# Kernel optimization log

Measured on AMD Instinct MI355X. Metric: run time of the kernel, lower is better.

## Reference

```python
import jax, jax.numpy as jnp
import numpy as np

B, W, C, H = 2, 2048, 1024, 16
K = C // H  # 64
LN_EPS = 1e-5


def setup_inputs() -> dict:
    key = jax.random.key(0)
    ks = jax.random.split(key, 8)
    return {
        "seq1": jax.random.normal(ks[0], (B, W, C), jnp.float32),
        "seq2": jax.random.normal(ks[1], (B, W, C), jnp.float32),
        "ln_gamma": jnp.ones((C,), jnp.float32),
        "ln_beta": jnp.zeros((C,), jnp.float32),
        "q_proj": jax.random.normal(ks[2], (H, C, K), jnp.float32) * 0.02,
        "k_proj": jax.random.normal(ks[3], (H, C, K), jnp.float32) * 0.02,
        "v_proj": jax.random.normal(ks[4], (H, C, K), jnp.float32) * 0.02,
        "mixer_w": jax.random.normal(ks[5], (C, C), jnp.float32) * 0.02,
        "mixer_b": jnp.zeros((C,), jnp.float32),
    }


def _layernorm(x, gamma, beta):
    mu = jnp.mean(x, axis=-1, keepdims=True)
    var = jnp.mean(jnp.square(x - mu), axis=-1, keepdims=True)
    return (x - mu) * jax.lax.rsqrt(var + LN_EPS) * gamma + beta


def reference(seq1, seq2, ln_gamma, ln_beta, q_proj, k_proj, v_proj, mixer_w, mixer_b):
    x1 = _layernorm(seq1, ln_gamma, ln_beta)  # [B,W,C]
    x2 = _layernorm(seq2, ln_gamma, ln_beta)
    # per-head projections: [B,W,C] x [H,C,K] -> [B,H,W,K]
    q = jnp.einsum("bwc,hck->bhwk", x1, q_proj)
    k = jnp.einsum("bwc,hck->bhwk", x2, k_proj)
    v = jnp.einsum("bwc,hck->bhwk", x2, v_proj)
    scores = jnp.einsum("bhqk,bhmk->bhqm", q, k) / jnp.sqrt(jnp.float32(K))
    # causal mask (is_decoder=True)
    causal = jnp.tril(jnp.ones((W, W), bool))
    scores = jnp.where(causal[None, None], scores, jnp.float32(-jnp.inf))
    probs = jax.nn.softmax(scores, axis=-1)
    out = jnp.einsum("bhqm,bhmk->bhqk", probs, v)  # [B,H,W,K]
    out = out.transpose(0, 2, 1, 3).reshape(B, W, C)  # [B,W,C]
    return out @ mixer_w.T + mixer_b
```

## Files before the change

kernel.cpp:

```cpp
#include <hip/hip_runtime.h>
#include <math.h>

#define B_ 2
#define W_ 2048
#define C_ 1024
#define H_ 16
#define K_ 64
#define LN_EPS 1e-5f

typedef __attribute__((ext_vector_type(8))) short short8;
typedef __attribute__((ext_vector_type(4))) float float4v;

#if __has_builtin(__builtin_amdgcn_exp2f)
#define EXP2(x) __builtin_amdgcn_exp2f(x)
#else
#define EXP2(x) exp2f(x)
#endif

__device__ inline unsigned short f2bf(float f) {
  unsigned u = __float_as_uint(f);
  u += 0x7fffu + ((u >> 16) & 1u);
  return (unsigned short)(u >> 16);
}

__device__ __forceinline__ void gload_lds16(const short* g, short* l) {
  __builtin_amdgcn_global_load_lds(
      (const __attribute__((address_space(1))) void*)g,
      (__attribute__((address_space(3))) void*)l, 16, 0, 0);
}

__device__ inline float block_sum(float val) {
  __shared__ float sb[4];
  #pragma unroll
  for (int o = 32; o > 0; o >>= 1) val += __shfl_down(val, o, 64);
  int lane = threadIdx.x & 63, wid = threadIdx.x >> 6;
  if (lane == 0) sb[wid] = val;
  __syncthreads();
  float r = sb[0] + sb[1] + sb[2] + sb[3];
  __syncthreads();
  return r;
}

__global__ __launch_bounds__(256) void ln_kernel(
    const float* __restrict__ seq1, const float* __restrict__ seq2,
    const float* __restrict__ gamma, const float* __restrict__ beta,
    short* __restrict__ x1b, short* __restrict__ x2b) {
  int row = blockIdx.x;
  const int nrows = B_ * W_;
  bool first = row < nrows;
  const float* src = first ? seq1 : seq2;
  short* dst = first ? x1b : x2b;
  int r = first ? row : row - nrows;

  const float4* p = (const float4*)(src + (size_t)r * C_);
  float4 v = p[threadIdx.x];
  float mean = block_sum(v.x + v.y + v.z + v.w) * (1.0f / C_);
  float dx = v.x - mean, dy = v.y - mean, dz = v.z - mean, dw = v.w - mean;
  float var = block_sum(dx * dx + dy * dy + dz * dz + dw * dw) * (1.0f / C_);
  float rstd = rsqrtf(var + LN_EPS);

  float4 g = ((const float4*)gamma)[threadIdx.x];
  float4 b = ((const float4*)beta)[threadIdx.x];
  uint2 o;
  o.x = (unsigned)f2bf(dx * rstd * g.x + b.x) |
        ((unsigned)f2bf(dy * rstd * g.y + b.y) << 16);
  o.y = (unsigned)f2bf(dz * rstd * g.z + b.z) |
        ((unsigned)f2bf(dw * rstd * g.w + b.w) << 16);
  ((uint2*)(dst + (size_t)r * C_))[threadIdx.x] = o;
}

__global__ __launch_bounds__(256) void wprep_proj_kernel(
    const float* __restrict__ qp, const float* __restrict__ kp,
    const float* __restrict__ vp,
    short* __restrict__ wqt, short* __restrict__ wkt, short* __restrict__ wvt) {
  int cb = blockIdx.x, h = blockIdx.y, which = blockIdx.z;
  const float* P = (which == 0 ? qp : (which == 1 ? kp : vp)) + (size_t)h * C_ * K_;
  short* Wt = (which == 0 ? wqt : (which == 1 ? wkt : wvt));
  float scale = (which == 0) ? 0.125f * 1.4426950408889634f : 1.0f;

  __shared__ float Ls[64][65];
  int t = threadIdx.x;
  {
    int cr = t >> 2, ks = (t & 3) * 16;
    const float* src = P + (size_t)(cb * 64 + cr) * K_ + ks;
    #pragma unroll
    for (int j = 0; j < 4; ++j) {
      float4 v = *(const float4*)(src + j * 4);
      Ls[cr][ks + j * 4 + 0] = v.x; Ls[cr][ks + j * 4 + 1] = v.y;
      Ls[cr][ks + j * 4 + 2] = v.z; Ls[cr][ks + j * 4 + 3] = v.w;
    }
  }
  __syncthreads();
  int kr = t >> 2, cs = (t & 3) * 16;
  unsigned u[8];
  #pragma unroll
  for (int i = 0; i < 8; ++i) {
    float a = Ls[cs + 2 * i][kr] * scale;
    float b = Ls[cs + 2 * i + 1][kr] * scale;
    u[i] = (unsigned)f2bf(a) | ((unsigned)f2bf(b) << 16);
  }
  short* dst = Wt + ((size_t)h * 64 + kr) * C_ + cb * 64 + cs;
  uint4 p0; p0.x = u[0]; p0.y = u[1]; p0.z = u[2]; p0.w = u[3];
  uint4 p1; p1.x = u[4]; p1.y = u[5]; p1.z = u[6]; p1.w = u[7];
  *(uint4*)dst = p0;
  *(uint4*)(dst + 8) = p1;
}

__global__ __launch_bounds__(256) void wprep_mix_kernel(
    const float* __restrict__ wm, short* __restrict__ wmb) {
  int gid = blockIdx.x * 256 + threadIdx.x;
  float4 v = ((const float4*)wm)[gid];
  uint2 o;
  o.x = (unsigned)f2bf(v.x) | ((unsigned)f2bf(v.y) << 16);
  o.y = (unsigned)f2bf(v.z) | ((unsigned)f2bf(v.w) << 16);
  ((uint2*)wmb)[gid] = o;
}

__device__ __forceinline__ void gemm_core(
    const short* __restrict__ A, const short* __restrict__ Bt,
    int arow0, int brow0, short* As, short* Bs, float4v acc[4][4]) {
  int tid = threadIdx.x;
  int wave = tid >> 6, lane = tid & 63;
  int lr = lane >> 3, lc = lane & 7;
  int sc = lc ^ lr;
  int wr = wave >> 1, wc = wave & 1;
  int lg = lane >> 4, ll = lane & 15;

  #pragma unroll
  for (int mi = 0; mi < 4; ++mi)
    #pragma unroll
    for (int ni = 0; ni < 4; ++ni) {
      acc[mi][ni][0] = 0.f; acc[mi][ni][1] = 0.f;
      acc[mi][ni][2] = 0.f; acc[mi][ni][3] = 0.f;
    }

  for (int k0 = 0; k0 < C_; k0 += 64) {
    __syncthreads();
    #pragma unroll
    for (int j = 0; j < 4; ++j) {
      int seg = wave * 4 + j;
      int r = seg * 8 + lr;
      gload_lds16(A + (size_t)(arow0 + r) * C_ + k0 + sc * 8, As + seg * 512);
      gload_lds16(Bt + (size_t)(brow0 + r) * C_ + k0 + sc * 8, Bs + seg * 512);
    }
    __syncthreads();
    #pragma unroll
    for (int kc = 0; kc < 2; ++kc) {
      int cc = kc * 4 + lg;
      short8 af[4], bf[4];
      #pragma unroll
      for (int mi = 0; mi < 4; ++mi) {
        int m = wr * 64 + mi * 16 + ll;
        af[mi] = *(const short8*)&As[m * 64 + ((cc ^ (m & 7)) << 3)];
      }
      #pragma unroll
      for (int ni = 0; ni < 4; ++ni) {
        int n = wc * 64 + ni * 16 + ll;
        bf[ni] = *(const short8*)&Bs[n * 64 + ((cc ^ (n & 7)) << 3)];
      }
      #pragma unroll
      for (int mi = 0; mi < 4; ++mi)
        #pragma unroll
        for (int ni = 0; ni < 4; ++ni)
          acc[mi][ni] = __builtin_amdgcn_mfma_f32_16x16x32_bf16(
              af[mi], bf[ni], acc[mi][ni], 0, 0, 0);
    }
  }
}

__device__ __forceinline__ void gemm_core64(
    const short* __restrict__ A, const short* __restrict__ Bt,
    int arow0, int brow0, short* As, short* Bs, float4v acc[2][4]) {
  int tid = threadIdx.x;
  int wave = tid >> 6, lane = tid & 63;
  int lr = lane >> 3, lc = lane & 7;
  int sc = lc ^ lr;
  int wr = wave >> 1, wc = wave & 1;
  int lg = lane >> 4, ll = lane & 15;

  #pragma unroll
  for (int mi = 0; mi < 2; ++mi)
    #pragma unroll
    for (int ni = 0; ni < 4; ++ni) {
      acc[mi][ni][0] = 0.f; acc[mi][ni][1] = 0.f;
      acc[mi][ni][2] = 0.f; acc[mi][ni][3] = 0.f;
    }

  for (int k0 = 0; k0 < C_; k0 += 64) {
    __syncthreads();
    #pragma unroll
    for (int j = 0; j < 2; ++j) {
      int seg = wave * 2 + j;
      int r = seg * 8 + lr;
      gload_lds16(A + (size_t)(arow0 + r) * C_ + k0 + sc * 8, As + seg * 512);
    }
    #pragma unroll
    for (int j = 0; j < 4; ++j) {
      int seg = wave * 4 + j;
      int r = seg * 8 + lr;
      gload_lds16(Bt + (size_t)(brow0 + r) * C_ + k0 + sc * 8, Bs + seg * 512);
    }
    __syncthreads();
    #pragma unroll
    for (int kc = 0; kc < 2; ++kc) {
      int cc = kc * 4 + lg;
      short8 af[2], bf[4];
      #pragma unroll
      for (int mi = 0; mi < 2; ++mi) {
        int m = wr * 32 + mi * 16 + ll;
        af[mi] = *(const short8*)&As[m * 64 + ((cc ^ (m & 7)) << 3)];
      }
      #pragma unroll
      for (int ni = 0; ni < 4; ++ni) {
        int n = wc * 64 + ni * 16 + ll;
        bf[ni] = *(const short8*)&Bs[n * 64 + ((cc ^ (n & 7)) << 3)];
      }
      #pragma unroll
      for (int mi = 0; mi < 2; ++mi)
        #pragma unroll
        for (int ni = 0; ni < 4; ++ni)
          acc[mi][ni] = __builtin_amdgcn_mfma_f32_16x16x32_bf16(
              af[mi], bf[ni], acc[mi][ni], 0, 0, 0);
    }
  }
}

__global__ __launch_bounds__(256, 3) void gemm_qkv_kernel(
    const short* __restrict__ x1b, const short* __restrict__ x2b,
    const short* __restrict__ wqt, const short* __restrict__ wkt,
    const short* __restrict__ wvt,
    short* __restrict__ qb, short* __restrict__ kb, short* __restrict__ vtb) {
  __shared__ short As[128 * 64], Bs[128 * 64];
  int z = blockIdx.z;
  const short *A, *Bt;
  int arow0, brow0;
  if (z == 0)      { A = x1b; Bt = wqt; arow0 = blockIdx.x * 128; brow0 = blockIdx.y * 128; }
  else if (z == 1) { A = x2b; Bt = wkt; arow0 = blockIdx.x * 128; brow0 = blockIdx.y * 128; }
  else             { A = wvt; Bt = x2b; arow0 = blockIdx.y * 128; brow0 = blockIdx.x * 128; }

  float4v acc[4][4];
  gemm_core(A, Bt, arow0, brow0, As, Bs, acc);

  int wave = threadIdx.x >> 6, lane = threadIdx.x & 63;
  int wr = wave >> 1, wc = wave & 1, lg = lane >> 4, ll = lane & 15;
  if (z <= 1) {
    short* O = (z == 0) ? qb : kb;
    #pragma unroll
    for (int mi = 0; mi < 4; ++mi)
      #pragma unroll
      for (int ni = 0; ni < 4; ++ni) {
        int n = brow0 + wc * 64 + ni * 16 + ll;
        int h = n >> 6, kk = n & 63;
        #pragma unroll
        for (int r2 = 0; r2 < 4; ++r2) {
          int m = arow0 + wr * 64 + mi * 16 + lg * 4 + r2;
          int b = m >> 11, w = m & (W_ - 1);
          O[((size_t)(b * H_ + h) * W_ + w) * K_ + kk] = (short)f2bf(acc[mi][ni][r2]);
        }
      }
  } else {
    #pragma unroll
    for (int mi = 0; mi < 4; ++mi)
      #pragma unroll
      for (int ni = 0; ni < 4; ++ni) {
        int n = brow0 + wc * 64 + ni * 16 + ll;
        int b = n >> 11, w = n & (W_ - 1);
        #pragma unroll
        for (int r2 = 0; r2 < 4; ++r2) {
          int m = arow0 + wr * 64 + mi * 16 + lg * 4 + r2;
          int h = m >> 6, kk = m & 63;
          vtb[((size_t)(b * H_ + h) * K_ + kk) * W_ + w] = (short)f2bf(acc[mi][ni][r2]);
        }
      }
  }
}

__global__ __launch_bounds__(256, 3) void gemm_mix_kernel(
    const short* __restrict__ attnb, const short* __restrict__ wmb,
    const float* __restrict__ bias, float* __restrict__ out) {
  __shared__ short As[64 * 64], Bs[128 * 64];
  int arow0 = blockIdx.x * 64, brow0 = blockIdx.y * 128;
  float4v acc[2][4];
  gemm_core64(attnb, wmb, arow0, brow0, As, Bs, acc);

  int wave = threadIdx.x >> 6, lane = threadIdx.x & 63;
  int wr = wave >> 1, wc = wave & 1, lg = lane >> 4, ll = lane & 15;
  #pragma unroll
  for (int mi = 0; mi < 2; ++mi)
    #pragma unroll
    for (int ni = 0; ni < 4; ++ni) {
      int n = brow0 + wc * 64 + ni * 16 + ll;
      float bv = bias[n];
      #pragma unroll
      for (int r2 = 0; r2 < 4; ++r2) {
        int m = arow0 + wr * 32 + mi * 16 + lg * 4 + r2;
        out[(size_t)m * C_ + n] = acc[mi][ni][r2] + bv;
      }
    }
}

__global__ __launch_bounds__(256, 3) void attn_mfma_kernel(
    const short* __restrict__ q, const short* __restrict__ k,
    const short* __restrict__ vt, short* __restrict__ out) {
  int bh = blockIdx.x;
  int b = bh >> 4, h = bh & 15;
  int s = blockIdx.y;
  int qt = (s < 16) ? (31 - s) : (s - 16);
  int wave = threadIdx.x >> 6;
  int lane = threadIdx.x & 63;
  int lg = lane >> 4, ll = lane & 15;

  __shared__ short Ks[2][64 * 64];
  __shared__ short Vs[2][64 * 64];
  __shared__ short Ps[4][16 * 72];

  const short* qp = q + (size_t)bh * W_ * K_;
  const short* kp = k + (size_t)bh * W_ * K_;
  const short* vb = vt + (size_t)bh * K_ * W_;

  int qrow = qt * 64 + wave * 16 + ll;
  short8 aq[2];
  #pragma unroll
  for (int kc = 0; kc < 2; ++kc)
    aq[kc] = *(const short8*)(qp + (size_t)qrow * K_ + kc * 32 + lg * 8);

  float4v o[4];
  #pragma unroll
  for (int ct = 0; ct < 4; ++ct) {
    o[ct][0] = 0.f; o[ct][1] = 0.f; o[ct][2] = 0.f; o[ct][3] = 0.f;
  }
  float m = -INFINITY, l = 0.f;

  int nkt = qt + 1;

  #define STAGE(kt, buf)                                                   \
    {                                                                      \
      const short* kbase = kp + (size_t)(kt) * 64 * K_;                    \
      const short* vbase = vb + (kt) * 64;                                 \
      _Pragma("unroll")                                                    \
      for (int j = 0; j < 2; ++j) {                                        \
        int sdx = j * 256 + (int)threadIdx.x;                              \
        int mm = sdx >> 3, c7 = sdx & 7;                                   \
        int gc = c7 ^ (mm & 7);                                            \
        gload_lds16(kbase + (size_t)mm * K_ + gc * 8, &Ks[buf][sdx * 8]);  \
        gload_lds16(vbase + (size_t)mm * W_ + gc * 8, &Vs[buf][sdx * 8]);  \
      }                                                                    \
    }

  STAGE(0, 0);
  for (int kt = 0; kt < nkt; ++kt) {
    int cur = kt & 1;
    if (kt + 1 < nkt) {
      STAGE(kt + 1, cur ^ 1);
      asm volatile("s_waitcnt vmcnt(4)\ns_barrier" ::: "memory");
    } else {
      asm volatile("s_waitcnt vmcnt(0)\ns_barrier" ::: "memory");
    }

    float4v st[4];
    #pragma unroll
    for (int nt = 0; nt < 4; ++nt) {
      st[nt][0] = 0.f; st[nt][1] = 0.f; st[nt][2] = 0.f; st[nt][3] = 0.f;
      int n = nt * 16 + ll;
      #pragma unroll
      for (int kc = 0; kc < 2; ++kc) {
        int cc = kc * 4 + lg;
        short8 bk = *(const short8*)&Ks[cur][n * 64 + ((cc ^ (n & 7)) << 3)];
        st[nt] = __builtin_amdgcn_mfma_f32_16x16x32_bf16(bk, aq[kc], st[nt], 0, 0, 0);
      }
    }
    short8 bv[4][2];
    #pragma unroll
    for (int ct = 0; ct < 4; ++ct) {
      int c = ct * 16 + ll;
      #pragma unroll
      for (int kc = 0; kc < 2; ++kc) {
        int cc = kc * 4 + lg;
        bv[ct][kc] = *(const short8*)&Vs[cur][c * 64 + ((cc ^ (c & 7)) << 3)];
      }
    }

    if (kt == qt) {
      #pragma unroll
      for (int nt = 0; nt < 4; ++nt) {
        int keyb = nt * 16 + lg * 4;
        #pragma unroll
        for (int r = 0; r < 4; ++r)
          if (keyb + r > wave * 16 + ll) st[nt][r] = -INFINITY;
      }
    }

    float mx0 = fmaxf(fmaxf(st[0][0], st[0][1]), fmaxf(st[0][2], st[0][3]));
    float mx1 = fmaxf(fmaxf(st[1][0], st[1][1]), fmaxf(st[1][2], st[1][3]));
    float mx2 = fmaxf(fmaxf(st[2][0], st[2][1]), fmaxf(st[2][2], st[2][3]));
    float mx3 = fmaxf(fmaxf(st[3][0], st[3][1]), fmaxf(st[3][2], st[3][3]));
    float lm = fmaxf(fmaxf(mx0, mx1), fmaxf(mx2, mx3));
    lm = fmaxf(lm, __shfl_xor(lm, 16, 64));
    lm = fmaxf(lm, __shfl_xor(lm, 32, 64));
    if (!__all(lm <= m + 8.f)) {
      float nm = fmaxf(m, lm);
      float al = EXP2(m - nm);
      m = nm;
      l *= al;
      #pragma unroll
      for (int ct = 0; ct < 4; ++ct) {
        o[ct][0] *= al; o[ct][1] *= al; o[ct][2] *= al; o[ct][3] *= al;
      }
    }
    float p[4][4];
    #pragma unroll
    for (int nt = 0; nt < 4; ++nt)
      #pragma unroll
      for (int r = 0; r < 4; ++r)
        p[nt][r] = EXP2(st[nt][r] - m);
    float s0 = (p[0][0] + p[0][1]) + (p[0][2] + p[0][3]);
    float s1 = (p[1][0] + p[1][1]) + (p[1][2] + p[1][3]);
    float s2 = (p[2][0] + p[2][1]) + (p[2][2] + p[2][3]);
    float s3 = (p[3][0] + p[3][1]) + (p[3][2] + p[3][3]);
    float ps = (s0 + s1) + (s2 + s3);
    ps += __shfl_xor(ps, 16, 64);
    ps += __shfl_xor(ps, 32, 64);
    l += ps;

    short* myP = &Ps[wave][ll * 72];
    #pragma unroll
    for (int nt = 0; nt < 4; ++nt) {
      uint2 w;
      w.x = (unsigned)f2bf(p[nt][0]) | ((unsigned)f2bf(p[nt][1]) << 16);
      w.y = (unsigned)f2bf(p[nt][2]) | ((unsigned)f2bf(p[nt][3]) << 16);
      *(uint2*)(myP + nt * 16 + lg * 4) = w;
    }
    __builtin_amdgcn_s_waitcnt(0xC07F);
    short8 bp0 = *(const short8*)(myP + lg * 8);
    short8 bp1 = *(const short8*)(myP + 32 + lg * 8);
    #pragma unroll
    for (int ct = 0; ct < 4; ++ct) {
      o[ct] = __builtin_amdgcn_mfma_f32_16x16x32_bf16(bv[ct][0], bp0, o[ct], 0, 0, 0);
      o[ct] = __builtin_amdgcn_mfma_f32_16x16x32_bf16(bv[ct][1], bp1, o[ct], 0, 0, 0);
    }
    asm volatile("s_waitcnt lgkmcnt(0)\ns_barrier" ::: "memory");
  }
  #undef STAGE

  float invl = 1.0f / l;
  size_t orow = ((size_t)(b * W_ + qrow)) * C_ + h * K_;
  #pragma unroll
  for (int ct = 0; ct < 4; ++ct) {
    uint2 w;
    w.x = (unsigned)f2bf(o[ct][0] * invl) | ((unsigned)f2bf(o[ct][1] * invl) << 16);
    w.y = (unsigned)f2bf(o[ct][2] * invl) | ((unsigned)f2bf(o[ct][3] * invl) << 16);
    *(uint2*)(out + orow + ct * 16 + lg * 4) = w;
  }
}

extern "C" void kernel_launch(void* const* d_in, const int* in_sizes, int n_in,
                              void* d_out, int out_size, void* d_ws, size_t ws_size,
                              hipStream_t stream) {
  const float* seq1  = (const float*)d_in[0];
  const float* seq2  = (const float*)d_in[1];
  const float* gamma = (const float*)d_in[2];
  const float* beta  = (const float*)d_in[3];
  const float* qp    = (const float*)d_in[4];
  const float* kp    = (const float*)d_in[5];
  const float* vp    = (const float*)d_in[6];
  const float* wm    = (const float*)d_in[7];
  const float* mb    = (const float*)d_in[8];
  float* out = (float*)d_out;

  char* ws = (char*)d_ws;
  const size_t NROW = (size_t)B_ * W_;
  const size_t XB = NROW * C_ * sizeof(short);
  const size_t WB = (size_t)C_ * C_ * sizeof(short);
  short* x1b = (short*)(ws);
  short* x2b = (short*)(ws + XB);
  short* qb  = (short*)(ws + 2 * XB);
  short* kb  = (short*)(ws + 3 * XB);
  short* vtb = (short*)(ws + 4 * XB);
  short* wqt = (short*)(ws + 5 * XB);
  short* wkt = (short*)(ws + 5 * XB + WB);
  short* wvt = (short*)(ws + 5 * XB + 2 * WB);
  short* wmb = (short*)(ws + 5 * XB + 3 * WB);
  short* attnb = (short*)(ws + 5 * XB + 4 * WB);

  wprep_proj_kernel<<<dim3(C_ / 64, H_, 3), dim3(256), 0, stream>>>(
      qp, kp, vp, wqt, wkt, wvt);
  wprep_mix_kernel<<<dim3(C_ * C_ / 1024), dim3(256), 0, stream>>>(wm, wmb);
  ln_kernel<<<dim3(2 * (unsigned)NROW), dim3(256), 0, stream>>>(
      seq1, seq2, gamma, beta, x1b, x2b);
  gemm_qkv_kernel<<<dim3(32, 8, 3), dim3(256), 0, stream>>>(
      x1b, x2b, wqt, wkt, wvt, qb, kb, vtb);
  attn_mfma_kernel<<<dim3(32, 32), dim3(256), 0, stream>>>(
      qb, kb, vtb, attnb);
  gemm_mix_kernel<<<dim3(64, 8), dim3(256), 0, stream>>>(attnb, wmb, mb, out);
}
```

Baseline: 192.7 us.

## Compute softmax row sums via MFMA with ones, add setprio and max3 reductions

Replaces the scalar per-tile row-sum and its cross-lane shuffles with two extra MFMAs that multiply a ones matrix by the bf16 probability tile, accumulating the denominator in matrix-core registers. Also wraps the MFMA sections in s_setprio to favour matrix issue across waves, and restructures the row-max into three-input max operations. The row sum now uses bf16-rounded probabilities, which matches what is fed to the PV product but changes numerics slightly, and it adds matrix-core work per tile.

```diff
diff --git a/kernel.cpp b/kernel.cpp
--- a/kernel.cpp
+++ b/kernel.cpp
@@ -21,6 +21,10 @@
   unsigned u = __float_as_uint(f);
   u += 0x7fffu + ((u >> 16) & 1u);
   return (unsigned short)(u >> 16);
+}
+
+__device__ inline float max3f(float a, float b, float c) {
+  return fmaxf(fmaxf(a, b), c);
 }
 
 __device__ __forceinline__ void gload_lds16(const short* g, short* l) {
@@ -324,12 +328,18 @@
   for (int kc = 0; kc < 2; ++kc)
     aq[kc] = *(const short8*)(qp + (size_t)qrow * K_ + kc * 32 + lg * 8);
 
+  short8 ones;
+  #pragma unroll
+  for (int i = 0; i < 8; ++i) ones[i] = (short)0x3F80;
+
   float4v o[4];
   #pragma unroll
   for (int ct = 0; ct < 4; ++ct) {
     o[ct][0] = 0.f; o[ct][1] = 0.f; o[ct][2] = 0.f; o[ct][3] = 0.f;
   }
-  float m = -INFINITY, l = 0.f;
+  float4v lsum;
+  lsum[0] = 0.f; lsum[1] = 0.f; lsum[2] = 0.f; lsum[3] = 0.f;
+  float m = -INFINITY;
 
   int nkt = qt + 1;
 
@@ -358,6 +368,7 @@
     }
 
     float4v st[4];
+    __builtin_amdgcn_s_setprio(1);
     #pragma unroll
     for (int nt = 0; nt < 4; ++nt) {
       st[nt][0] = 0.f; st[nt][1] = 0.f; st[nt][2] = 0.f; st[nt][3] = 0.f;
@@ -369,6 +380,8 @@
         st[nt] = __builtin_amdgcn_mfma_f32_16x16x32_bf16(bk, aq[kc], st[nt], 0, 0, 0);
       }
     }
+    __builtin_amdgcn_s_setprio(0);
+
     short8 bv[4][2];
     #pragma unroll
     for (int ct = 0; ct < 4; ++ct) {
@@ -390,37 +403,31 @@
       }
     }
 
-    float mx0 = fmaxf(fmaxf(st[0][0], st[0][1]), fmaxf(st[0][2], st[0][3]));
-    float mx1 = fmaxf(fmaxf(st[1][0], st[1][1]), fmaxf(st[1][2], st[1][3]));
-    float mx2 = fmaxf(fmaxf(st[2][0], st[2][1]), fmaxf(st[2][2], st[2][3]));
-    float mx3 = fmaxf(fmaxf(st[3][0], st[3][1]), fmaxf(st[3][2], st[3][3]));
-    float lm = fmaxf(fmaxf(mx0, mx1), fmaxf(mx2, mx3));
+    float ma = max3f(st[0][0], st[0][1], st[0][2]);
+    float mb = max3f(st[0][3], st[1][0], st[1][1]);
+    float mc = max3f(st[1][2], st[1][3], st[2][0]);
+    float md = max3f(st[2][1], st[2][2], st[2][3]);
+    float me = max3f(st[3][0], st[3][1], st[3][2]);
+    float lm = fmaxf(max3f(ma, mb, mc), max3f(md, me, st[3][3]));
     lm = fmaxf(lm, __shfl_xor(lm, 16, 64));
     lm = fmaxf(lm, __shfl_xor(lm, 32, 64));
     if (!__all(lm <= m + 8.f)) {
       float nm = fmaxf(m, lm);
       float al = EXP2(m - nm);
       m = nm;
-      l *= al;
+      lsum[0] *= al; lsum[1] *= al; lsum[2] *= al; lsum[3] *= al;
       #pragma unroll
       for (int ct = 0; ct < 4; ++ct) {
         o[ct][0] *= al; o[ct][1] *= al; o[ct][2] *= al; o[ct][3] *= al;
       }
     }
+
     float p[4][4];
     #pragma unroll
     for (int nt = 0; nt < 4; ++nt)
       #pragma unroll
       for (int r = 0; r < 4; ++r)
         p[nt][r] = EXP2(st[nt][r] - m);
-    float s0 = (p[0][0] + p[0][1]) + (p[0][2] + p[0][3]);
-    float s1 = (p[1][0] + p[1][1]) + (p[1][2] + p[1][3]);
-    float s2 = (p[2][0] + p[2][1]) + (p[2][2] + p[2][3]);
-    float s3 = (p[3][0] + p[3][1]) + (p[3][2] + p[3][3]);
-    float ps = (s0 + s1) + (s2 + s3);
-    ps += __shfl_xor(ps, 16, 64);
-    ps += __shfl_xor(ps, 32, 64);
-    l += ps;
 
     short* myP = &Ps[wave][ll * 72];
     #pragma unroll
@@ -433,16 +440,21 @@
     __builtin_amdgcn_s_waitcnt(0xC07F);
     short8 bp0 = *(const short8*)(myP + lg * 8);
     short8 bp1 = *(const short8*)(myP + 32 + lg * 8);
+
+    __builtin_amdgcn_s_setprio(1);
+    lsum = __builtin_amdgcn_mfma_f32_16x16x32_bf16(ones, bp0, lsum, 0, 0, 0);
+    lsum = __builtin_amdgcn_mfma_f32_16x16x32_bf16(ones, bp1, lsum, 0, 0, 0);
     #pragma unroll
     for (int ct = 0; ct < 4; ++ct) {
       o[ct] = __builtin_amdgcn_mfma_f32_16x16x32_bf16(bv[ct][0], bp0, o[ct], 0, 0, 0);
       o[ct] = __builtin_amdgcn_mfma_f32_16x16x32_bf16(bv[ct][1], bp1, o[ct], 0, 0, 0);
     }
+    __builtin_amdgcn_s_setprio(0);
     asm volatile("s_waitcnt lgkmcnt(0)\ns_barrier" ::: "memory");
   }
   #undef STAGE
 
-  float invl = 1.0f / l;
+  float invl = 1.0f / lsum[0];
   size_t orow = ((size_t)(b * W_ + qrow)) * C_ + h * K_;
   #pragma unroll
   for (int ct = 0; ct < 4; ++ct) {
```

Measured after the change: 197.6 us. 2.5% more time.
